# Kernel tuning notes

Hardware: AMD Instinct MI355X
Metric: run time of the kernel (lower is better)

## Reference

```python
import jax, jax.numpy as jnp
import numpy as np

NUM_USERS = 100000
NUM_ITEMS = 50000
NUM_EDGES = 1000000
EMB_DIM = 64


def setup_inputs() -> dict:
    key = jax.random.key(0)
    k1, k2, k3, k4, k5, k6 = jax.random.split(key, 6)
    return {
        "user_emb": jax.random.normal(k1, (NUM_USERS, EMB_DIM), dtype=jnp.float32),
        "item_emb": jax.random.normal(k2, (NUM_ITEMS, EMB_DIM), dtype=jnp.float32),
        "u_sw": jax.random.uniform(k3, (NUM_USERS, 1), dtype=jnp.float32),
        "i_sw": jax.random.uniform(k4, (NUM_ITEMS, 1), dtype=jnp.float32),
        "edge_src_user": jax.random.randint(k5, (NUM_EDGES,), 0, NUM_USERS, dtype=jnp.int32),
        "edge_dst_item": jax.random.randint(k6, (NUM_EDGES,), 0, NUM_ITEMS, dtype=jnp.int32),
    }


def _segment_mean(feat_src, src_idx, dst_idx, num_dst, inv_deg):
    # gather source node features onto edges, sum-reduce at destinations, divide by degree
    s = jax.ops.segment_sum(feat_src[src_idx], dst_idx, num_segments=num_dst)
    return s * inv_deg


def reference(user_emb, item_emb, u_sw, i_sw, edge_src_user, edge_dst_item):
    ones = jnp.ones((edge_src_user.shape[0],), dtype=user_emb.dtype)
    deg_i = jax.ops.segment_sum(ones, edge_dst_item, num_segments=NUM_ITEMS)
    deg_u = jax.ops.segment_sum(ones, edge_src_user, num_segments=NUM_USERS)
    # DGL mean gives 0 for zero-degree nodes
    inv_deg_i = jnp.where(deg_i > 0, 1.0 / jnp.maximum(deg_i, 1.0), 0.0)[:, None]
    inv_deg_u = jnp.where(deg_u > 0, 1.0 / jnp.maximum(deg_u, 1.0), 0.0)[:, None]

    def one_round(u, i):
        # 'like': user -> item mean aggregation; 'rev_like': item -> user
        new_i = _segment_mean(u, edge_src_user, edge_dst_item, NUM_ITEMS, inv_deg_i)
        new_u = _segment_mean(i, edge_dst_item, edge_src_user, NUM_USERS, inv_deg_u)
        return new_u + u * u_sw, new_i + i * i_sw

    u, i = one_round(user_emb, item_emb)
    u, i = one_round(u, i)
    return (u, i)
```

## Files before the change

### kernel.cpp

```cpp
#include <hip/hip_runtime.h>
#include <hip/hip_fp16.h>

#define NU 100000
#define NI 50000
#define NE 1000000
#define D  64
#define NBI 196
#define NBU 391
#define NB_TOT (NBI + NBU)
#define CHUNK 4096

__device__ __forceinline__ unsigned short f2h(float f) {
    return __half_as_ushort(__float2half(f));
}
__device__ __forceinline__ float h2f(unsigned short h) {
    return __half2float(__ushort_as_half(h));
}

__global__ void k_bhist_cvt(const int* __restrict__ esrc, const int* __restrict__ edst,
                            int* __restrict__ bcnt,
                            const float* __restrict__ ue, const float* __restrict__ ie,
                            unsigned short* __restrict__ u0h, unsigned short* __restrict__ i0h) {
    __shared__ int h[NB_TOT];
    for (int b = threadIdx.x; b < NB_TOT; b += blockDim.x) h[b] = 0;
    __syncthreads();
    int gt = blockIdx.x * blockDim.x + threadIdx.x;
    int gs = gridDim.x * blockDim.x;
    for (int e = gt; e < NE; e += gs) {
        atomicAdd(&h[edst[e] >> 8], 1);
        atomicAdd(&h[NBI + (esrc[e] >> 8)], 1);
    }
    const float4* uf = (const float4*)ue;
    ushort4* uh = (ushort4*)u0h;
    for (int i = gt; i < NU * (D / 4); i += gs) {
        float4 v = uf[i];
        ushort4 o; o.x = f2h(v.x); o.y = f2h(v.y); o.z = f2h(v.z); o.w = f2h(v.w);
        uh[i] = o;
    }
    const float4* if4 = (const float4*)ie;
    ushort4* ih = (ushort4*)i0h;
    for (int i = gt; i < NI * (D / 4); i += gs) {
        float4 v = if4[i];
        ushort4 o; o.x = f2h(v.x); o.y = f2h(v.y); o.z = f2h(v.z); o.w = f2h(v.w);
        ih[i] = o;
    }
    __syncthreads();
    for (int b = threadIdx.x; b < NB_TOT; b += blockDim.x) {
        int v = h[b];
        if (v) atomicAdd(&bcnt[b], v);
    }
}

__global__ void k_bscan_both(const int* __restrict__ bcnt,
                             int* __restrict__ bbase_i, int* __restrict__ gcur_i,
                             int* __restrict__ bbase_u, int* __restrict__ gcur_u) {
    __shared__ int s[512];
    int tid = threadIdx.x;
    const int* in = (blockIdx.x == 0) ? bcnt : bcnt + NBI;
    int nb        = (blockIdx.x == 0) ? NBI : NBU;
    int* bbase    = (blockIdx.x == 0) ? bbase_i : bbase_u;
    int* gcur     = (blockIdx.x == 0) ? gcur_i : gcur_u;
    int v = (tid < nb) ? in[tid] : 0;
    s[tid] = v;
    __syncthreads();
    for (int o = 1; o < 512; o <<= 1) {
        int t = (tid >= o) ? s[tid - o] : 0;
        __syncthreads();
        s[tid] += t;
        __syncthreads();
    }
    if (tid < nb) { int ex = s[tid] - v; bbase[tid] = ex; gcur[tid] = ex; }
    if (tid == 0) bbase[nb] = NE;
}

__global__ void k_part_both(const int* __restrict__ esrc, const int* __restrict__ edst,
                            int* __restrict__ gcur_i, int* __restrict__ gcur_u,
                            unsigned int* __restrict__ rec_i, unsigned int* __restrict__ rec_u) {
    __shared__ int cnt_i[NBI], gb_i[NBI], cnt_u[NBU], gb_u[NBU];
    int tid = threadIdx.x;
    for (int b = tid; b < NBI; b += 256) cnt_i[b] = 0;
    for (int b = tid; b < NBU; b += 256) cnt_u[b] = 0;
    __syncthreads();
    int base = blockIdx.x * CHUNK;
    int dd[16], uu[16], ki[16], ku[16];
#pragma unroll
    for (int k = 0; k < 16; k++) {
        int j = base + tid + k * 256;
        dd[k] = -1;
        if (j < NE) {
            dd[k] = edst[j]; uu[k] = esrc[j];
            ki[k] = atomicAdd(&cnt_i[dd[k] >> 8], 1);
            ku[k] = atomicAdd(&cnt_u[uu[k] >> 8], 1);
        }
    }
    __syncthreads();
    for (int b = tid; b < NBI; b += 256) { int v = cnt_i[b]; if (v) gb_i[b] = atomicAdd(&gcur_i[b], v); }
    for (int b = tid; b < NBU; b += 256) { int v = cnt_u[b]; if (v) gb_u[b] = atomicAdd(&gcur_u[b], v); }
    __syncthreads();
#pragma unroll
    for (int k = 0; k < 16; k++) {
        if (dd[k] >= 0) {
            rec_i[gb_i[dd[k] >> 8] + ki[k]] = ((unsigned int)(dd[k] & 255) << 17) | (unsigned int)uu[k];
            rec_u[gb_u[uu[k] >> 8] + ku[k]] = ((unsigned int)(uu[k] & 255) << 17) | (unsigned int)dd[k];
        }
    }
}

__global__ void k_local_both(const unsigned int* __restrict__ rec_i, const unsigned int* __restrict__ rec_u,
                             const int* __restrict__ bbase_i, const int* __restrict__ bbase_u,
                             int* __restrict__ rp_i, int* __restrict__ rp_u,
                             int* __restrict__ col_i, int* __restrict__ col_u) {
    __shared__ int cnt[256];
    __shared__ int off[256];
    int tid = threadIdx.x;
    int t = blockIdx.x;
    bool item = t < NBI;
    int b = item ? t : t - NBI;
    const unsigned int* rec = item ? rec_i : rec_u;
    const int* bb = item ? bbase_i : bbase_u;
    int* rp  = item ? rp_i : rp_u;
    int* col = item ? col_i : col_u;
    int nn   = item ? NI : NU;
    int beg = bb[b], end = bb[b + 1];
    cnt[tid] = 0;
    __syncthreads();
    for (int j = beg + tid; j < end; j += 256)
        atomicAdd(&cnt[rec[j] >> 17], 1);
    __syncthreads();
    int v = cnt[tid];
    off[tid] = v;
    __syncthreads();
    for (int o = 1; o < 256; o <<= 1) {
        int tv = (tid >= o) ? off[tid - o] : 0;
        __syncthreads();
        off[tid] += tv;
        __syncthreads();
    }
    int ex = off[tid] - v;
    int node = b * 256 + tid;
    if (node <= nn) rp[node] = beg + ex;
    cnt[tid] = ex;
    __syncthreads();
    for (int j = beg + tid; j < end; j += 256) {
        unsigned int r = rec[j];
        int p = atomicAdd(&cnt[r >> 17], 1);
        col[beg + p] = (int)(r & 0x1FFFF);
    }
}

template<bool WF, bool WH>
__device__ __forceinline__ void agg_h(const unsigned short* __restrict__ feat,
        const unsigned short* selfh, const float* __restrict__ sw,
        const int* __restrict__ rp, const int* __restrict__ cols,
        float* __restrict__ outf, unsigned short* outh,
        int n, int li, int lb) {
    int beg = rp[n], end = rp[n + 1];
    float ax = 0.f, ay = 0.f, az = 0.f, aw = 0.f;
    for (int j0 = beg; j0 < end; j0 += 16) {
        int cv = (j0 + li < end) ? cols[j0 + li] : 0;
        int nj = end - j0;
        ushort4 h[16];
#pragma unroll
        for (int j = 0; j < 16; j++) {
            int c = __shfl(cv, lb + j, 64);
            h[j] = *(const ushort4*)(feat + (size_t)c * D + li * 4);
        }
#pragma unroll
        for (int j = 0; j < 16; j++) {
            float w = (j < nj) ? 1.0f : 0.0f;
            ax = fmaf(w, h2f(h[j].x), ax);
            ay = fmaf(w, h2f(h[j].y), ay);
            az = fmaf(w, h2f(h[j].z), az);
            aw = fmaf(w, h2f(h[j].w), aw);
        }
    }
    int dgr = end - beg;
    float inv = (dgr > 0) ? (1.0f / (float)dgr) : 0.0f;
    float swv = sw[n];
    ushort4 s4 = *(const ushort4*)(selfh + (size_t)n * D + li * 4);
    float rx = ax * inv + h2f(s4.x) * swv;
    float ry = ay * inv + h2f(s4.y) * swv;
    float rz = az * inv + h2f(s4.z) * swv;
    float rw = aw * inv + h2f(s4.w) * swv;
    if (WH) {
        ushort4 o; o.x = f2h(rx); o.y = f2h(ry); o.z = f2h(rz); o.w = f2h(rw);
        *(ushort4*)(outh + (size_t)n * D + li * 4) = o;
    }
    if (WF) {
        float4 o; o.x = rx; o.y = ry; o.z = rz; o.w = rw;
        *(float4*)(outf + (size_t)n * D + li * 4) = o;
    }
}

__global__ void k_agg_r1i(const unsigned short* __restrict__ u0h, const unsigned short* __restrict__ i0h,
                          const float* __restrict__ i_sw,
                          const int* __restrict__ rp_i, const int* __restrict__ col_i,
                          unsigned short* __restrict__ i1h) {
    int g  = (blockIdx.x * blockDim.x + threadIdx.x) >> 4;
    if (g >= NI) return;
    agg_h<false, true>(u0h, i0h, i_sw, rp_i, col_i, nullptr, i1h, g, threadIdx.x & 15, threadIdx.x & 48);
}

__global__ void k_agg_r1u(const unsigned short* __restrict__ i0h, const unsigned short* u0h,
                          const float* __restrict__ u_sw,
                          const int* __restrict__ rp_u, const int* __restrict__ col_u,
                          unsigned short* u1h) {
    int g  = (blockIdx.x * blockDim.x + threadIdx.x) >> 4;
    if (g >= NU) return;
    agg_h<false, true>(i0h, u0h, u_sw, rp_u, col_u, nullptr, u1h, g, threadIdx.x & 15, threadIdx.x & 48);
}

__global__ void k_agg_r2i(const unsigned short* __restrict__ u1h, const unsigned short* __restrict__ i1h,
                          const float* __restrict__ i_sw,
                          const int* __restrict__ rp_i, const int* __restrict__ col_i,
                          float* __restrict__ out_i) {
    int g  = (blockIdx.x * blockDim.x + threadIdx.x) >> 4;
    if (g >= NI) return;
    agg_h<true, false>(u1h, i1h, i_sw, rp_i, col_i, out_i, nullptr, g, threadIdx.x & 15, threadIdx.x & 48);
}

__global__ void k_agg_r2u(const unsigned short* __restrict__ i1h, const unsigned short* __restrict__ u1h,
                          const float* __restrict__ u_sw,
                          const int* __restrict__ rp_u, const int* __restrict__ col_u,
                          float* __restrict__ out_u) {
    int g  = (blockIdx.x * blockDim.x + threadIdx.x) >> 4;
    if (g >= NU) return;
    agg_h<true, false>(i1h, u1h, u_sw, rp_u, col_u, out_u, nullptr, g, threadIdx.x & 15, threadIdx.x & 48);
}

extern "C" void kernel_launch(void* const* d_in, const int* in_sizes, int n_in,
                              void* d_out, int out_size, void* d_ws, size_t ws_size,
                              hipStream_t stream) {
    const float* user_emb = (const float*)d_in[0];
    const float* item_emb = (const float*)d_in[1];
    const float* u_sw     = (const float*)d_in[2];
    const float* i_sw     = (const float*)d_in[3];
    const int*   esrc     = (const int*)d_in[4];
    const int*   edst     = (const int*)d_in[5];

    float* out_u = (float*)d_out;
    float* out_i = out_u + NU * D;

    int* bcnt    = (int*)d_ws;
    int* bbase_i = bcnt + NB_TOT;
    int* bbase_u = bbase_i + NBI + 1;
    int* gcur_i  = bbase_u + NBU + 1;
    int* gcur_u  = gcur_i + NBI;
    int* rp_i    = gcur_u + NBU;
    int* rp_u    = rp_i + NI + 1;
    int* col_i   = rp_u + NU + 1;
    int* col_u   = col_i + NE;
    uintptr_t pa = ((uintptr_t)(col_u + NE) + 15) & ~(uintptr_t)15;
    unsigned short* u0h = (unsigned short*)pa;
    unsigned short* i0h = u0h + (size_t)NU * D;
    uintptr_t pc = (uintptr_t)(i0h + (size_t)NI * D);
    unsigned int* rec_i = (unsigned int*)pc;
    unsigned int* rec_u = rec_i + NE;
    unsigned short* i1h = (unsigned short*)pc;
    unsigned short* u1h = u0h;

    hipMemsetAsync(bcnt, 0, NB_TOT * sizeof(int), stream);

    const int B = 256;

    k_bhist_cvt<<<1024, B, 0, stream>>>(esrc, edst, bcnt, user_emb, item_emb, u0h, i0h);
    k_bscan_both<<<2, 512, 0, stream>>>(bcnt, bbase_i, gcur_i, bbase_u, gcur_u);
    k_part_both<<<(NE + CHUNK - 1) / CHUNK, B, 0, stream>>>(esrc, edst, gcur_i, gcur_u, rec_i, rec_u);
    k_local_both<<<NB_TOT, B, 0, stream>>>(rec_i, rec_u, bbase_i, bbase_u, rp_i, rp_u, col_i, col_u);

    k_agg_r1i<<<(NI * 16) / B, B, 0, stream>>>(u0h, i0h, i_sw, rp_i, col_i, i1h);
    k_agg_r1u<<<(NU * 16) / B, B, 0, stream>>>(i0h, u0h, u_sw, rp_u, col_u, u1h);
    k_agg_r2i<<<(NI * 16) / B, B, 0, stream>>>(u1h, i1h, i_sw, rp_i, col_i, out_i);
    k_agg_r2u<<<(NU * 16) / B, B, 0, stream>>>(i1h, u1h, u_sw, rp_u, col_u, out_u);
}
```

Baseline: 277.1 us.

## Merge item/user aggregation launches per round and shrink partition chunk

Fuses the item and user aggregation kernels of each round into a single launch covering both node sets. For round one this needs a separate u1h buffer, so it is only used when the workspace is large enough, with a fallback to the two old launches. The partition chunk is halved to get more blocks with less register state, and the self-feature and weight loads are moved ahead of the neighbor loop so their latency overlaps the gathers. The fused launches remove a launch gap and a tail-drain per round, at the cost of extra workspace and branch divergence at the item/user boundary block.

After: 278.8 us. About the same (+0.6%).

```diff
diff --git a/kernel.cpp b/kernel.cpp
--- a/kernel.cpp
+++ b/kernel.cpp
@@ -8,7 +8,8 @@
 #define NBI 196
 #define NBU 391
 #define NB_TOT (NBI + NBU)
-#define CHUNK 4096
+#define CHUNK 2048
+#define PART_K (CHUNK / 256)
 
 __device__ __forceinline__ unsigned short f2h(float f) {
     return __half_as_ushort(__float2half(f));
@@ -82,9 +83,9 @@
     for (int b = tid; b < NBU; b += 256) cnt_u[b] = 0;
     __syncthreads();
     int base = blockIdx.x * CHUNK;
-    int dd[16], uu[16], ki[16], ku[16];
+    int dd[PART_K], uu[PART_K], ki[PART_K], ku[PART_K];
 #pragma unroll
-    for (int k = 0; k < 16; k++) {
+    for (int k = 0; k < PART_K; k++) {
         int j = base + tid + k * 256;
         dd[k] = -1;
         if (j < NE) {
@@ -98,7 +99,7 @@
     for (int b = tid; b < NBU; b += 256) { int v = cnt_u[b]; if (v) gb_u[b] = atomicAdd(&gcur_u[b], v); }
     __syncthreads();
 #pragma unroll
-    for (int k = 0; k < 16; k++) {
+    for (int k = 0; k < PART_K; k++) {
         if (dd[k] >= 0) {
             rec_i[gb_i[dd[k] >> 8] + ki[k]] = ((unsigned int)(dd[k] & 255) << 17) | (unsigned int)uu[k];
             rec_u[gb_u[uu[k] >> 8] + ku[k]] = ((unsigned int)(uu[k] & 255) << 17) | (unsigned int)dd[k];
@@ -155,6 +156,8 @@
         float* __restrict__ outf, unsigned short* outh,
         int n, int li, int lb) {
     int beg = rp[n], end = rp[n + 1];
+    float swv = sw[n];
+    ushort4 s4 = *(const ushort4*)(selfh + (size_t)n * D + li * 4);
     float ax = 0.f, ay = 0.f, az = 0.f, aw = 0.f;
     for (int j0 = beg; j0 < end; j0 += 16) {
         int cv = (j0 + li < end) ? cols[j0 + li] : 0;
@@ -176,8 +179,6 @@
     }
     int dgr = end - beg;
     float inv = (dgr > 0) ? (1.0f / (float)dgr) : 0.0f;
-    float swv = sw[n];
-    ushort4 s4 = *(const ushort4*)(selfh + (size_t)n * D + li * 4);
     float rx = ax * inv + h2f(s4.x) * swv;
     float ry = ay * inv + h2f(s4.y) * swv;
     float rz = az * inv + h2f(s4.z) * swv;
@@ -192,40 +193,53 @@
     }
 }
 
-__global__ void k_agg_r1i(const unsigned short* __restrict__ u0h, const unsigned short* __restrict__ i0h,
-                          const float* __restrict__ i_sw,
-                          const int* __restrict__ rp_i, const int* __restrict__ col_i,
-                          unsigned short* __restrict__ i1h) {
+__global__ __launch_bounds__(256) void k_agg_r1(
+        const unsigned short* __restrict__ u0h, const unsigned short* __restrict__ i0h,
+        const float* __restrict__ u_sw, const float* __restrict__ i_sw,
+        const int* __restrict__ rp_i, const int* __restrict__ rp_u,
+        const int* __restrict__ col_i, const int* __restrict__ col_u,
+        unsigned short* __restrict__ i1h, unsigned short* __restrict__ u1h) {
+    int g  = (blockIdx.x * blockDim.x + threadIdx.x) >> 4;
+    int li = threadIdx.x & 15;
+    int lb = threadIdx.x & 48;
+    if (g < NI)
+        agg_h<false, true>(u0h, i0h, i_sw, rp_i, col_i, nullptr, i1h, g, li, lb);
+    else
+        agg_h<false, true>(i0h, u0h, u_sw, rp_u, col_u, nullptr, u1h, g - NI, li, lb);
+}
+
+__global__ __launch_bounds__(256) void k_agg_r1i(
+        const unsigned short* __restrict__ u0h, const unsigned short* __restrict__ i0h,
+        const float* __restrict__ i_sw,
+        const int* __restrict__ rp_i, const int* __restrict__ col_i,
+        unsigned short* __restrict__ i1h) {
     int g  = (blockIdx.x * blockDim.x + threadIdx.x) >> 4;
     if (g >= NI) return;
     agg_h<false, true>(u0h, i0h, i_sw, rp_i, col_i, nullptr, i1h, g, threadIdx.x & 15, threadIdx.x & 48);
 }
-
-__global__ void k_agg_r1u(const unsigned short* __restrict__ i0h, const unsigned short* u0h,
-                          const float* __restrict__ u_sw,
-                          const int* __restrict__ rp_u, const int* __restrict__ col_u,
-                          unsigned short* u1h) {
+__global__ __launch_bounds__(256) void k_agg_r1u(
+        const unsigned short* __restrict__ i0h, const unsigned short* u0h,
+        const float* __restrict__ u_sw,
+        const int* __restrict__ rp_u, const int* __restrict__ col_u,
+        unsigned short* u1h) {
     int g  = (blockIdx.x * blockDim.x + threadIdx.x) >> 4;
     if (g >= NU) return;
     agg_h<false, true>(i0h, u0h, u_sw, rp_u, col_u, nullptr, u1h, g, threadIdx.x & 15, threadIdx.x & 48);
 }
 
-__global__ void k_agg_r2i(const unsigned short* __restrict__ u1h, const unsigned short* __restrict__ i1h,
-                          const float* __restrict__ i_sw,
-                          const int* __restrict__ rp_i, const int* __restrict__ col_i,
-                          float* __restrict__ out_i) {
+__global__ __launch_bounds__(256) void k_agg_r2(
+        const unsigned short* __restrict__ u1h, const unsigned short* __restrict__ i1h,
+        const float* __restrict__ u_sw, const float* __restrict__ i_sw,
+        const int* __restrict__ rp_i, const int* __restrict__ rp_u,
+        const int* __restrict__ col_i, const int* __restrict__ col_u,
+        float* __restrict__ out_i, float* __restrict__ out_u) {
     int g  = (blockIdx.x * blockDim.x + threadIdx.x) >> 4;
-    if (g >= NI) return;
-    agg_h<true, false>(u1h, i1h, i_sw, rp_i, col_i, out_i, nullptr, g, threadIdx.x & 15, threadIdx.x & 48);
-}
-
-__global__ void k_agg_r2u(const unsigned short* __restrict__ i1h, const unsigned short* __restrict__ u1h,
-                          const float* __restrict__ u_sw,
-                          const int* __restrict__ rp_u, const int* __restrict__ col_u,
-                          float* __restrict__ out_u) {
-    int g  = (blockIdx.x * blockDim.x + threadIdx.x) >> 4;
-    if (g >= NU) return;
-    agg_h<true, false>(i1h, u1h, u_sw, rp_u, col_u, out_u, nullptr, g, threadIdx.x & 15, threadIdx.x & 48);
+    int li = threadIdx.x & 15;
+    int lb = threadIdx.x & 48;
+    if (g < NI)
+        agg_h<true, false>(u1h, i1h, i_sw, rp_i, col_i, out_i, nullptr, g, li, lb);
+    else
+        agg_h<true, false>(i1h, u1h, u_sw, rp_u, col_u, out_u, nullptr, g - NI, li, lb);
 }
 
 extern "C" void kernel_launch(void* const* d_in, const int* in_sizes, int n_in,
@@ -257,7 +271,11 @@
     unsigned int* rec_i = (unsigned int*)pc;
     unsigned int* rec_u = rec_i + NE;
     unsigned short* i1h = (unsigned short*)pc;
-    unsigned short* u1h = u0h;
+    uintptr_t pd = (uintptr_t)(rec_u + NE);
+    unsigned short* u1h_big = (unsigned short*)pd;
+    size_t need = (pd + (size_t)NU * D * sizeof(unsigned short)) - (uintptr_t)d_ws;
+    bool bigws = ws_size >= need;
+    unsigned short* u1h = bigws ? u1h_big : u0h;
 
     hipMemsetAsync(bcnt, 0, NB_TOT * sizeof(int), stream);
 
@@ -268,8 +286,15 @@
     k_part_both<<<(NE + CHUNK - 1) / CHUNK, B, 0, stream>>>(esrc, edst, gcur_i, gcur_u, rec_i, rec_u);
     k_local_both<<<NB_TOT, B, 0, stream>>>(rec_i, rec_u, bbase_i, bbase_u, rp_i, rp_u, col_i, col_u);
 
-    k_agg_r1i<<<(NI * 16) / B, B, 0, stream>>>(u0h, i0h, i_sw, rp_i, col_i, i1h);
-    k_agg_r1u<<<(NU * 16) / B, B, 0, stream>>>(i0h, u0h, u_sw, rp_u, col_u, u1h);
-    k_agg_r2i<<<(NI * 16) / B, B, 0, stream>>>(u1h, i1h, i_sw, rp_i, col_i, out_i);
-    k_agg_r2u<<<(NU * 16) / B, B, 0, stream>>>(i1h, u1h, u_sw, rp_u, col_u, out_u);
-}
+    if (bigws) {
+        k_agg_r1<<<((NI + NU) * 16) / B, B, 0, stream>>>(u0h, i0h, u_sw, i_sw,
+                                                         rp_i, rp_u, col_i, col_u,
+                                                         i1h, u1h);
+    } else {
+        k_agg_r1i<<<(NI * 16) / B, B, 0, stream>>>(u0h, i0h, i_sw, rp_i, col_i, i1h);
+        k_agg_r1u<<<(NU * 16) / B, B, 0, stream>>>(i0h, u0h, u_sw, rp_u, col_u, u1h);
+    }
+    k_agg_r2<<<((NI + NU) * 16) / B, B, 0, stream>>>(u1h, i1h, u_sw, i_sw,
+                                                     rp_i, rp_u, col_i, col_u,
+                                                     out_i, out_u);
+}
```
